# Performance work log

Hardware: AMD Instinct MI355X
Metric: run time of the kernel (lower is better)

Reference implementation:

```python
import jax, jax.numpy as jnp
from jax import lax
import numpy as np

B, S, N, F, H = 8, 64, 256, 16, 16
C = N * H  # temporal conv channels = 4096
ALPHA = 0.2
EPS = 1e-5
NEG = -9e15


def setup_inputs() -> dict:
    key = jax.random.key(0)
    ks = jax.random.split(key, 10)
    x = jax.random.normal(ks[0], (B, S, N, F), dtype=jnp.float32)
    adj = jax.random.normal(ks[1], (N, N), dtype=jnp.float32)
    W = jax.random.normal(ks[2], (F, H), dtype=jnp.float32) * (1.414 / np.sqrt(F))
    a = jax.random.normal(ks[3], (2 * H,), dtype=jnp.float32) * (1.414 / np.sqrt(2 * H))
    a1, a2 = a[:H], a[H:]
    conv_w = jax.random.normal(ks[4], (C, C, 3), dtype=jnp.float32) * (1.0 / np.sqrt(C * 3))
    conv_b = jnp.zeros((C,), dtype=jnp.float32)
    bn_gamma = jnp.ones((C,), dtype=jnp.float32)
    bn_beta = jnp.zeros((C,), dtype=jnp.float32)
    bn_mean = jnp.zeros((C,), dtype=jnp.float32)
    bn_var = jnp.ones((C,), dtype=jnp.float32)
    ln_gamma = jnp.ones((H,), dtype=jnp.float32)
    ln_beta = jnp.zeros((H,), dtype=jnp.float32)
    return {"x": x, "adj": adj, "W": W, "a1": a1, "a2": a2,
            "conv_w": conv_w, "conv_b": conv_b,
            "bn_gamma": bn_gamma, "bn_beta": bn_beta,
            "bn_mean": bn_mean, "bn_var": bn_var,
            "ln_gamma": ln_gamma, "ln_beta": ln_beta}


def reference(x, adj, W, a1, a2, conv_w, conv_b, bn_gamma, bn_beta, bn_mean, bn_var, ln_gamma, ln_beta):
    b, s, n, f = x.shape
    h = W.shape[1]
    # --- GAT, batched over all timesteps (eval mode: dropout is identity) ---
    Wh = jnp.einsum('bsnf,fh->bsnh', x, W)            # (B,S,N,H)
    # e_ij = LeakyReLU(a1.Wh_i + a2.Wh_j), equivalent to concat-then-matmul
    f1 = jnp.einsum('bsnh,h->bsn', Wh, a1)
    f2 = jnp.einsum('bsnh,h->bsn', Wh, a2)
    e = jax.nn.leaky_relu(f1[..., :, None] + f2[..., None, :], ALPHA)  # (B,S,N,N)
    e = jnp.where(adj > 0, e, NEG)
    attn = jax.nn.softmax(e, axis=-1)
    spatial = jnp.einsum('bsij,bsjh->bsih', attn, Wh)  # (B,S,N,H)
    # --- temporal conv over seq dim, channels = N*H ---
    t = spatial.reshape(b, s, n * h).transpose(0, 2, 1)  # (B,C,S)
    y = lax.conv_general_dilated(t, conv_w, window_strides=(1,), padding=[(1, 1)],
                                 dimension_numbers=('NCH', 'OIH', 'NCH'))
    y = y + conv_b[None, :, None]
    # BatchNorm1d in eval mode
    y = (y - bn_mean[None, :, None]) / jnp.sqrt(bn_var + EPS)[None, :, None]
    y = y * bn_gamma[None, :, None] + bn_beta[None, :, None]
    y = jax.nn.relu(y)
    temp = y.transpose(0, 2, 1).reshape(b, s, n, h)
    # residual is identity since in_features == hidden_dim
    out = temp + x
    # LayerNorm over last dim
    mu = out.mean(-1, keepdims=True)
    var = out.var(-1, keepdims=True)
    out = (out - mu) / jnp.sqrt(var + EPS) * ln_gamma + ln_beta
    return out
```

## Files before the change

kernel.cpp:

```cpp
#include <hip/hip_runtime.h>
#include <stdint.h>

#define ALPHA 0.2f
#define EPSV  1e-5f

typedef unsigned short u16;
typedef unsigned int   u32;
typedef unsigned long long u64;
typedef __bf16 bf16x8 __attribute__((ext_vector_type(8)));
typedef __bf16 bf16x2 __attribute__((ext_vector_type(2)));
typedef float  f32x4  __attribute__((ext_vector_type(4)));

#define NB 8
#define NS 64
#define NN 256
#define NF 16
#define NH 16
#define NC 4096
#define NK 12288
#define NP 512

__device__ __forceinline__ u16 f2b(float f){
  u32 u = __float_as_uint(f);
  u32 r = u + 0x7fffu + ((u>>16)&1u);
  return (u16)(r>>16);
}
__device__ __forceinline__ u32 pack2(float a, float b){ return (u32)f2b(a) | ((u32)f2b(b)<<16); }
__device__ __forceinline__ void un2(u32 v, float& lo, float& hi){
  lo = __uint_as_float(v<<16); hi = __uint_as_float(v & 0xffff0000u);
}
__device__ __forceinline__ void gld16(void* lds, const void* g){
  __builtin_amdgcn_global_load_lds((const __attribute__((address_space(1))) u32*)g,
                                   (__attribute__((address_space(3))) u32*)lds, 16, 0, 0);
}
__device__ __forceinline__ uint4 cvt8(f32x4 a, f32x4 b){
  union { uint4 u; bf16x2 h[4]; } r;
  r.h[0] = (bf16x2){(__bf16)a[0], (__bf16)a[1]};
  r.h[1] = (bf16x2){(__bf16)a[2], (__bf16)a[3]};
  r.h[2] = (bf16x2){(__bf16)b[0], (__bf16)b[1]};
  r.h[3] = (bf16x2){(__bf16)b[2], (__bf16)b[3]};
  return r.u;
}

__global__ __launch_bounds__(256) void k_adj(const float* __restrict__ adj,
                                             u64* __restrict__ am){
  int w = threadIdx.x>>6, l = threadIdx.x&63;
  int row = blockIdx.x*4 + w;
  #pragma unroll
  for(int g=0;g<4;g++){
    float v = adj[(size_t)row*NN + g*64 + l];
    u64 m = __ballot(v > 0.f);
    if(l==0) am[row*4+g] = m;
  }
}

__global__ __launch_bounds__(256) void k_attn(
    const float* __restrict__ x, const float* __restrict__ W,
    const float* __restrict__ a1, const float* __restrict__ a2,
    const u64* __restrict__ am, u16* __restrict__ Bt){
  __shared__ __align__(16) float Ws[NF][NH];
  __shared__ float a1s[NH], a2s[NH];
  __shared__ __align__(16) float Whs[NN][NH];
  __shared__ float f2s[NN];
  int t = threadIdx.x, bs = blockIdx.x;
  int b = bs>>6, s = bs&63;
  Ws[t>>4][t&15] = W[t];
  if(t<NH){ a1s[t]=a1[t]; a2s[t]=a2[t]; }
  u64 mg[4];
  #pragma unroll
  for(int g=0;g<4;g++) mg[g] = am[t*4+g];
  __syncthreads();

  const float* xp = x + ((size_t)bs*NN + t)*NF;
  float xr[16];
  #pragma unroll
  for(int g=0;g<4;g++) *(f32x4*)&xr[g*4] = ((const f32x4*)xp)[g];
  float wh[16];
  #pragma unroll
  for(int h=0;h<16;h++) wh[h]=0.f;
  #pragma unroll
  for(int f=0;f<16;f++){
    float xf = xr[f];
    #pragma unroll
    for(int h=0;h<16;h++) wh[h] = fmaf(xf, Ws[f][h], wh[h]);
  }
  float fi=0.f, s2=0.f;
  #pragma unroll
  for(int h=0;h<16;h++){ fi=fmaf(wh[h],a1s[h],fi); s2=fmaf(wh[h],a2s[h],s2); }
  #pragma unroll
  for(int g=0;g<4;g++) ((f32x4*)Whs[t])[g] = *(f32x4*)&wh[g*4];
  f2s[t] = s2;
  __syncthreads();

  float den = 0.f;
  f32x4 a0={0,0,0,0}, a1v={0,0,0,0}, a2v={0,0,0,0}, a3v={0,0,0,0};
  #pragma unroll
  for(int g=0;g<4;g++){
    u64 mm = mg[g];
    for(int jj=0;jj<64;jj++){
      int j = g*64+jj;
      float e = fi + f2s[j];
      e = e > 0.f ? e : ALPHA*e;
      float p = ((mm>>jj)&1ull) ? __expf(e) : 0.f;
      den += p;
      const f32x4* wr = (const f32x4*)Whs[j];
      a0 += wr[0]*p; a1v += wr[1]*p; a2v += wr[2]*p; a3v += wr[3]*p;
    }
  }
  float inv = 1.f/fmaxf(den, 1e-30f);
  float vals[16];
  *(f32x4*)&vals[0]  = a0*inv;  *(f32x4*)&vals[4]  = a1v*inv;
  *(f32x4*)&vals[8]  = a2v*inv; *(f32x4*)&vals[12] = a3v*inv;

  #pragma unroll
  for(int k=0;k<3;k++){
    int cs = s + 1 - k;
    if(cs >= 0 && cs < NS){
      size_t base = ((size_t)(b*NS+cs))*NK + (size_t)t*48 + k;
      #pragma unroll
      for(int h=0;h<16;h++) Bt[base + h*3] = f2b(vals[h]);
    }
  }
  if(s == 0){
    size_t base = ((size_t)(b*NS))*NK + (size_t)t*48;
    #pragma unroll
    for(int h=0;h<16;h++) Bt[base + h*3] = 0;
  }
  if(s == NS-1){
    size_t base = ((size_t)(b*NS+NS-1))*NK + (size_t)t*48 + 2;
    #pragma unroll
    for(int h=0;h<16;h++) Bt[base + h*3] = 0;
  }
}

__global__ __launch_bounds__(256) void k_gemm(
    const u16* __restrict__ Abt, const float* __restrict__ Bwf,
    u16* __restrict__ yp, int kchunk){
  __shared__ __align__(16) u16 As0[128*32];
  __shared__ __align__(16) u16 As1[128*32];
  __shared__ __align__(16) u16 Bs0[128*32];
  __shared__ __align__(16) u16 Bs1[128*32];
  int t = threadIdx.x;
  int id = blockIdx.x;
  int xr_ = id & 7, q0 = id >> 3;
  int mI = q0 & 3, nhi = q0 >> 2;
  int m0 = mI*128, n0 = (nhi*8 + xr_)*128;
  int kbeg = blockIdx.y*kchunk;
  f32x4 acc[4][4];
  #pragma unroll
  for(int i=0;i<4;i++)
    #pragma unroll
    for(int j=0;j<4;j++) acc[i][j] = (f32x4){0,0,0,0};

  int l = t&63, w = t>>6;
  int wm = (w&1)*64, wn = (w>>1)*64;
  int q = l>>4, r16 = l&15;

  int c0 = t, c1 = t+256;
  const u16*   ga0 = Abt + (size_t)(m0 + (c0>>2))*NK + (c0&3)*8;
  const u16*   ga1 = Abt + (size_t)(m0 + (c1>>2))*NK + (c1&3)*8;
  const float* gb0 = Bwf + (size_t)(n0 + (c0>>2))*NK + (c0&3)*8;
  const float* gb1 = Bwf + (size_t)(n0 + (c1>>2))*NK + (c1&3)*8;
  u16 *la00 = As0 + c0*8, *la01 = As0 + c1*8;
  u16 *la10 = As1 + c0*8, *la11 = As1 + c1*8;
  u16 *lb00 = Bs0 + c0*8, *lb01 = Bs0 + c1*8;
  u16 *lb10 = Bs1 + c0*8, *lb11 = Bs1 + c1*8;

  for(int kk=0; kk<kchunk; kk+=64){
    int k0 = kbeg + kk;
    f32x4 v00a = *(const f32x4*)(gb0 + k0);
    f32x4 v00b = *(const f32x4*)(gb0 + k0 + 4);
    f32x4 v01a = *(const f32x4*)(gb1 + k0);
    f32x4 v01b = *(const f32x4*)(gb1 + k0 + 4);
    f32x4 v10a = *(const f32x4*)(gb0 + k0 + 32);
    f32x4 v10b = *(const f32x4*)(gb0 + k0 + 36);
    f32x4 v11a = *(const f32x4*)(gb1 + k0 + 32);
    f32x4 v11b = *(const f32x4*)(gb1 + k0 + 36);
    uint4 w00 = cvt8(v00a, v00b);
    uint4 w01 = cvt8(v01a, v01b);
    uint4 w10 = cvt8(v10a, v10b);
    uint4 w11 = cvt8(v11a, v11b);
    __syncthreads();
    gld16(la00, ga0 + k0);      gld16(la01, ga1 + k0);
    gld16(la10, ga0 + k0 + 32); gld16(la11, ga1 + k0 + 32);
    *(uint4*)lb00 = w00; *(uint4*)lb01 = w01;
    *(uint4*)lb10 = w10; *(uint4*)lb11 = w11;
    __syncthreads();
    {
      bf16x8 af[4], bfr[4];
      #pragma unroll
      for(int mt=0;mt<4;mt++) af[mt]  = *(const bf16x8*)(As0 + (wm+mt*16+r16)*32 + q*8);
      #pragma unroll
      for(int nt=0;nt<4;nt++) bfr[nt] = *(const bf16x8*)(Bs0 + (wn+nt*16+r16)*32 + q*8);
      #pragma unroll
      for(int mt=0;mt<4;mt++)
        #pragma unroll
        for(int nt=0;nt<4;nt++)
          acc[mt][nt] = __builtin_amdgcn_mfma_f32_16x16x32_bf16(af[mt], bfr[nt], acc[mt][nt], 0,0,0);
    }
    {
      bf16x8 af[4], bfr[4];
      #pragma unroll
      for(int mt=0;mt<4;mt++) af[mt]  = *(const bf16x8*)(As1 + (wm+mt*16+r16)*32 + q*8);
      #pragma unroll
      for(int nt=0;nt<4;nt++) bfr[nt] = *(const bf16x8*)(Bs1 + (wn+nt*16+r16)*32 + q*8);
      #pragma unroll
      for(int mt=0;mt<4;mt++)
        #pragma unroll
        for(int nt=0;nt<4;nt++)
          acc[mt][nt] = __builtin_amdgcn_mfma_f32_16x16x32_bf16(af[mt], bfr[nt], acc[mt][nt], 0,0,0);
    }
  }
  u16* op = yp + (size_t)blockIdx.y*NP*NC;
  #pragma unroll
  for(int mt=0;mt<4;mt++)
    #pragma unroll
    for(int nt=0;nt<4;nt++)
      #pragma unroll
      for(int rr=0;rr<4;rr++){
        int m = m0 + wm + mt*16 + q*4 + rr;
        int n = n0 + wn + nt*16 + r16;
        op[(size_t)m*NC + n] = f2b(acc[mt][nt][rr]);
      }
}

__global__ __launch_bounds__(256) void k_post(
    const u16* __restrict__ yp, int nparts,
    const float* __restrict__ x,
    const float* __restrict__ cb, const float* __restrict__ bg,
    const float* __restrict__ bb, const float* __restrict__ bm,
    const float* __restrict__ bv, const float* __restrict__ lg,
    const float* __restrict__ lb, float* __restrict__ out){
  int n = threadIdx.x, bs = blockIdx.x;
  float v[16];
  #pragma unroll
  for(int h=0;h<16;h++) v[h]=0.f;
  for(int p=0;p<nparts;p++){
    const u16* pp = yp + (size_t)p*NP*NC + (size_t)bs*NC + n*16;
    uint4 u0 = ((const uint4*)pp)[0];
    uint4 u1 = ((const uint4*)pp)[1];
    float lo, hi;
    un2(u0.x,lo,hi); v[0]+=lo;  v[1]+=hi;
    un2(u0.y,lo,hi); v[2]+=lo;  v[3]+=hi;
    un2(u0.z,lo,hi); v[4]+=lo;  v[5]+=hi;
    un2(u0.w,lo,hi); v[6]+=lo;  v[7]+=hi;
    un2(u1.x,lo,hi); v[8]+=lo;  v[9]+=hi;
    un2(u1.y,lo,hi); v[10]+=lo; v[11]+=hi;
    un2(u1.z,lo,hi); v[12]+=lo; v[13]+=hi;
    un2(u1.w,lo,hi); v[14]+=lo; v[15]+=hi;
  }
  const float* xp = x + ((size_t)bs*NN + n)*NH;
  float xr[16];
  #pragma unroll
  for(int g=0;g<4;g++) *(f32x4*)&xr[g*4] = ((const f32x4*)xp)[g];

  float mu = 0.f;
  #pragma unroll
  for(int h=0;h<16;h++){
    int co = n*16 + h;
    float t1 = v[h] + cb[co];
    t1 = (t1 - bm[co]) * (1.f/sqrtf(bv[co] + EPSV));
    t1 = t1 * bg[co] + bb[co];
    t1 = fmaxf(t1, 0.f);
    t1 += xr[h];
    v[h] = t1; mu += t1;
  }
  mu *= (1.f/16.f);
  float var = 0.f;
  #pragma unroll
  for(int h=0;h<16;h++){ float d = v[h]-mu; var = fmaf(d,d,var); }
  var *= (1.f/16.f);
  float rs = 1.f/sqrtf(var + EPSV);
  float* op = out + ((size_t)bs*NN + n)*NH;
  #pragma unroll
  for(int h=0;h<16;h++) op[h] = (v[h]-mu)*rs*lg[h] + lb[h];
}

extern "C" void kernel_launch(void* const* d_in, const int* in_sizes, int n_in,
                              void* d_out, int out_size, void* d_ws, size_t ws_size,
                              hipStream_t stream){
  const float* x   = (const float*)d_in[0];
  const float* adj = (const float*)d_in[1];
  const float* W   = (const float*)d_in[2];
  const float* a1  = (const float*)d_in[3];
  const float* a2  = (const float*)d_in[4];
  const float* cw  = (const float*)d_in[5];
  const float* cb  = (const float*)d_in[6];
  const float* bg  = (const float*)d_in[7];
  const float* bb  = (const float*)d_in[8];
  const float* bm  = (const float*)d_in[9];
  const float* bv  = (const float*)d_in[10];
  const float* lg  = (const float*)d_in[11];
  const float* lb  = (const float*)d_in[12];
  float* out = (float*)d_out;

  char* ws = (char*)d_ws;
  const size_t AM_OFF = 0;
  const size_t BT_OFF = AM_OFF + (size_t)NN*4*8;
  const size_t YP_OFF = BT_OFF + (size_t)NP*NK*2;
  const size_t ypb    = (size_t)NP*NC*2;
  int P = 1;
  if(ws_size >= YP_OFF + 8*ypb)      P = 8;
  else if(ws_size >= YP_OFF + 4*ypb) P = 4;
  else if(ws_size >= YP_OFF + 2*ypb) P = 2;

  u64*   am  = (u64*)  (ws + AM_OFF);
  u16*   Bt  = (u16*)  (ws + BT_OFF);
  u16*   yp  = (u16*)  (ws + YP_OFF);

  hipLaunchKernelGGL(k_adj,  dim3(64),    dim3(256), 0, stream, adj, am);
  hipLaunchKernelGGL(k_attn, dim3(NP),    dim3(256), 0, stream, x,W,a1,a2,am,Bt);
  hipLaunchKernelGGL(k_gemm, dim3(128,P), dim3(256), 0, stream, Bt, cw, yp, NK/P);
  hipLaunchKernelGGL(k_post, dim3(NP),    dim3(256), 0, stream, yp,P,x,cb,bg,bb,bm,bv,lg,lb,out);
}
```

Before: 429.3 us.

## Pre-convert conv weights to bf16 and use padded spatial layout as implicit im2col

```diff
diff --git a/kernel.cpp b/kernel.cpp
--- a/kernel.cpp
+++ b/kernel.cpp
@@ -19,6 +19,7 @@
 #define NC 4096
 #define NK 12288
 #define NP 512
+#define SROW 66
 
 __device__ __forceinline__ u16 f2b(float f){
   u32 u = __float_as_uint(f);
@@ -43,7 +44,8 @@
 }
 
 __global__ __launch_bounds__(256) void k_adj(const float* __restrict__ adj,
-                                             u64* __restrict__ am){
+                                             u64* __restrict__ am,
+                                             uint4* __restrict__ spz){
   int w = threadIdx.x>>6, l = threadIdx.x&63;
   int row = blockIdx.x*4 + w;
   #pragma unroll
@@ -52,9 +54,181 @@
     u64 m = __ballot(v > 0.f);
     if(l==0) am[row*4+g] = m;
   }
+  if(spz){
+    int g = blockIdx.x*256 + threadIdx.x;
+    if(g < 8192){
+      int r = g>>9;
+      int b = r>>1;
+      size_t prow = (size_t)b*SROW + ((r&1) ? (SROW-1) : 0);
+      spz[prow*512 + (g&511)] = (uint4){0,0,0,0};
+    }
+  }
+}
+
+__global__ __launch_bounds__(256) void k_cw(const float* __restrict__ cw,
+                                            u16* __restrict__ Bw){
+  __shared__ __align__(16) float rs_[NK];
+  int t = threadIdx.x, co = blockIdx.x;
+  const float* src = cw + (size_t)co*NK;
+  #pragma unroll
+  for(int i=0;i<12;i++)
+    gld16(rs_ + (i*256 + t)*4, src + (i*256 + t)*4);
+  __syncthreads();
+  u16* dst = Bw + (size_t)co*NK;
+  #pragma unroll
+  for(int c=0;c<6;c++){
+    int o  = c*2048 + t*8;
+    int k  = o>>12, ci = o & 4095;
+    const float* p = rs_ + ci*3 + k;
+    union { uint4 u; u16 h[8]; } r;
+    #pragma unroll
+    for(int j=0;j<8;j++) r.h[j] = f2b(p[j*3]);
+    *(uint4*)(dst + o) = r.u;
+  }
 }
 
 __global__ __launch_bounds__(256) void k_attn(
+    const float* __restrict__ x, const float* __restrict__ W,
+    const float* __restrict__ a1, const float* __restrict__ a2,
+    const u64* __restrict__ am, u16* __restrict__ Sp){
+  __shared__ __align__(16) float Ws[NF][NH];
+  __shared__ float a1s[NH], a2s[NH];
+  __shared__ __align__(16) float Whs[NN][NH];
+  __shared__ float f2s[NN];
+  int t = threadIdx.x, bs = blockIdx.x;
+  int b = bs>>6, s = bs&63;
+  Ws[t>>4][t&15] = W[t];
+  if(t<NH){ a1s[t]=a1[t]; a2s[t]=a2[t]; }
+  u64 mg[4];
+  #pragma unroll
+  for(int g=0;g<4;g++) mg[g] = am[t*4+g];
+  __syncthreads();
+
+  const float* xp = x + ((size_t)bs*NN + t)*NF;
+  float xr[16];
+  #pragma unroll
+  for(int g=0;g<4;g++) *(f32x4*)&xr[g*4] = ((const f32x4*)xp)[g];
+  float wh[16];
+  #pragma unroll
+  for(int h=0;h<16;h++) wh[h]=0.f;
+  #pragma unroll
+  for(int f=0;f<16;f++){
+    float xf = xr[f];
+    #pragma unroll
+    for(int h=0;h<16;h++) wh[h] = fmaf(xf, Ws[f][h], wh[h]);
+  }
+  float fi=0.f, s2=0.f;
+  #pragma unroll
+  for(int h=0;h<16;h++){ fi=fmaf(wh[h],a1s[h],fi); s2=fmaf(wh[h],a2s[h],s2); }
+  #pragma unroll
+  for(int g=0;g<4;g++) ((f32x4*)Whs[t])[g] = *(f32x4*)&wh[g*4];
+  f2s[t] = s2;
+  __syncthreads();
+
+  float den = 0.f;
+  f32x4 a0={0,0,0,0}, a1v={0,0,0,0}, a2v={0,0,0,0}, a3v={0,0,0,0};
+  #pragma unroll
+  for(int g=0;g<4;g++){
+    u64 mm = mg[g];
+    for(int jj=0;jj<64;jj++){
+      int j = g*64+jj;
+      float e = fi + f2s[j];
+      e = e > 0.f ? e : ALPHA*e;
+      float p = ((mm>>jj)&1ull) ? __expf(e) : 0.f;
+      den += p;
+      const f32x4* wr = (const f32x4*)Whs[j];
+      a0 += wr[0]*p; a1v += wr[1]*p; a2v += wr[2]*p; a3v += wr[3]*p;
+    }
+  }
+  float inv = 1.f/fmaxf(den, 1e-30f);
+  f32x4 o0 = a0*inv, o1 = a1v*inv, o2 = a2v*inv, o3 = a3v*inv;
+
+  uint4 w0 = cvt8(o0,o1), w1 = cvt8(o2,o3);
+  uint4* op = (uint4*)(Sp + ((size_t)(b*SROW + s + 1))*NC) + t*2;
+  op[0] = w0; op[1] = w1;
+}
+
+__global__ __launch_bounds__(256) void k_gemm(
+    const u16* __restrict__ Asp, const u16* __restrict__ Bw,
+    u16* __restrict__ yp, int kchunk){
+  __shared__ __align__(16) u16 As0[128*32];
+  __shared__ __align__(16) u16 As1[128*32];
+  __shared__ __align__(16) u16 Bs0[128*32];
+  __shared__ __align__(16) u16 Bs1[128*32];
+  int t = threadIdx.x;
+  int id = blockIdx.x;
+  int xr_ = id & 7, q0 = id >> 3;
+  int mI = q0 & 3, nhi = q0 >> 2;
+  int m0 = mI*128, n0 = (nhi*8 + xr_)*128;
+  int kbeg = blockIdx.y*kchunk;
+  f32x4 acc[4][4];
+  #pragma unroll
+  for(int i=0;i<4;i++)
+    #pragma unroll
+    for(int j=0;j<4;j++) acc[i][j] = (f32x4){0,0,0,0};
+
+  int l = t&63, w = t>>6;
+  int wm = (w&1)*64, wn = (w>>1)*64;
+  int q = l>>4, r16 = l&15;
+
+  int c0 = t, c1 = t+256;
+  int mA0 = m0 + (c0>>2), mA1 = m0 + (c1>>2);
+  const u16* ga0 = Asp + (size_t)((mA0>>6)*SROW + (mA0&63))*NC + (c0&3)*8;
+  const u16* ga1 = Asp + (size_t)((mA1>>6)*SROW + (mA1&63))*NC + (c1&3)*8;
+  const u16* gb0 = Bw  + (size_t)(n0 + (c0>>2))*NK + (c0&3)*8;
+  const u16* gb1 = Bw  + (size_t)(n0 + (c1>>2))*NK + (c1&3)*8;
+  u16 *la00 = As0 + c0*8, *la01 = As0 + c1*8;
+  u16 *la10 = As1 + c0*8, *la11 = As1 + c1*8;
+  u16 *lb00 = Bs0 + c0*8, *lb01 = Bs0 + c1*8;
+  u16 *lb10 = Bs1 + c0*8, *lb11 = Bs1 + c1*8;
+
+  for(int kk=0; kk<kchunk; kk+=64){
+    int k0 = kbeg + kk;
+    __syncthreads();
+    gld16(la00, ga0 + k0);      gld16(la01, ga1 + k0);
+    gld16(la10, ga0 + k0 + 32); gld16(la11, ga1 + k0 + 32);
+    gld16(lb00, gb0 + k0);      gld16(lb01, gb1 + k0);
+    gld16(lb10, gb0 + k0 + 32); gld16(lb11, gb1 + k0 + 32);
+    __syncthreads();
+    {
+      bf16x8 af[4], bfr[4];
+      #pragma unroll
+      for(int mt=0;mt<4;mt++) af[mt]  = *(const bf16x8*)(As0 + (wm+mt*16+r16)*32 + q*8);
+      #pragma unroll
+      for(int nt=0;nt<4;nt++) bfr[nt] = *(const bf16x8*)(Bs0 + (wn+nt*16+r16)*32 + q*8);
+      #pragma unroll
+      for(int mt=0;mt<4;mt++)
+        #pragma unroll
+        for(int nt=0;nt<4;nt++)
+          acc[mt][nt] = __builtin_amdgcn_mfma_f32_16x16x32_bf16(af[mt], bfr[nt], acc[mt][nt], 0,0,0);
+    }
+    {
+      bf16x8 af[4], bfr[4];
+      #pragma unroll
+      for(int mt=0;mt<4;mt++) af[mt]  = *(const bf16x8*)(As1 + (wm+mt*16+r16)*32 + q*8);
+      #pragma unroll
+      for(int nt=0;nt<4;nt++) bfr[nt] = *(const bf16x8*)(Bs1 + (wn+nt*16+r16)*32 + q*8);
+      #pragma unroll
+      for(int mt=0;mt<4;mt++)
+        #pragma unroll
+        for(int nt=0;nt<4;nt++)
+          acc[mt][nt] = __builtin_amdgcn_mfma_f32_16x16x32_bf16(af[mt], bfr[nt], acc[mt][nt], 0,0,0);
+    }
+  }
+  u16* op = yp + (size_t)blockIdx.y*NP*NC;
+  #pragma unroll
+  for(int mt=0;mt<4;mt++)
+    #pragma unroll
+    for(int nt=0;nt<4;nt++)
+      #pragma unroll
+      for(int rr=0;rr<4;rr++){
+        int m = m0 + wm + mt*16 + q*4 + rr;
+        int n = n0 + wn + nt*16 + r16;
+        op[(size_t)m*NC + n] = f2b(acc[mt][nt][rr]);
+      }
+}
+
+__global__ __launch_bounds__(256) void k_attn_s(
     const float* __restrict__ x, const float* __restrict__ W,
     const float* __restrict__ a1, const float* __restrict__ a2,
     const u64* __restrict__ am, u16* __restrict__ Bt){
@@ -133,7 +307,7 @@
   }
 }
 
-__global__ __launch_bounds__(256) void k_gemm(
+__global__ __launch_bounds__(256) void k_gemm_f(
     const u16* __restrict__ Abt, const float* __restrict__ Bwf,
     u16* __restrict__ yp, int kchunk){
   __shared__ __align__(16) u16 As0[128*32];
@@ -295,21 +469,43 @@
   float* out = (float*)d_out;
 
   char* ws = (char*)d_ws;
-  const size_t AM_OFF = 0;
-  const size_t BT_OFF = AM_OFF + (size_t)NN*4*8;
-  const size_t YP_OFF = BT_OFF + (size_t)NP*NK*2;
-  const size_t ypb    = (size_t)NP*NC*2;
-  int P = 1;
-  if(ws_size >= YP_OFF + 8*ypb)      P = 8;
-  else if(ws_size >= YP_OFF + 4*ypb) P = 4;
-  else if(ws_size >= YP_OFF + 2*ypb) P = 2;
-
-  u64*   am  = (u64*)  (ws + AM_OFF);
-  u16*   Bt  = (u16*)  (ws + BT_OFF);
-  u16*   yp  = (u16*)  (ws + YP_OFF);
-
-  hipLaunchKernelGGL(k_adj,  dim3(64),    dim3(256), 0, stream, adj, am);
-  hipLaunchKernelGGL(k_attn, dim3(NP),    dim3(256), 0, stream, x,W,a1,a2,am,Bt);
-  hipLaunchKernelGGL(k_gemm, dim3(128,P), dim3(256), 0, stream, Bt, cw, yp, NK/P);
-  hipLaunchKernelGGL(k_post, dim3(NP),    dim3(256), 0, stream, yp,P,x,cb,bg,bb,bm,bv,lg,lb,out);
-}
+  const size_t ypb = (size_t)NP*NC*2;
+
+  const size_t SP_OFF  = 8192;
+  const size_t SP_SZ   = (size_t)NB*SROW*NC*2;
+  const size_t BW_OFF  = SP_OFF + SP_SZ;
+  const size_t BW_SZ   = (size_t)NC*NK*2;
+  const size_t YP_OFF2 = BW_OFF + BW_SZ;
+
+  u64* am = (u64*)ws;
+
+  int P2 = 0;
+  if(ws_size >= YP_OFF2 + 8*ypb)      P2 = 8;
+  else if(ws_size >= YP_OFF2 + 4*ypb) P2 = 4;
+  else if(ws_size >= YP_OFF2 + 2*ypb) P2 = 2;
+  else if(ws_size >= YP_OFF2 + 1*ypb) P2 = 1;
+
+  if(P2){
+    u16* Sp = (u16*)(ws + SP_OFF);
+    u16* Bw = (u16*)(ws + BW_OFF);
+    u16* yp = (u16*)(ws + YP_OFF2);
+    hipLaunchKernelGGL(k_adj,  dim3(64),      dim3(256), 0, stream, adj, am, (uint4*)Sp);
+    hipLaunchKernelGGL(k_cw,   dim3(NC),      dim3(256), 0, stream, cw, Bw);
+    hipLaunchKernelGGL(k_attn, dim3(NP),      dim3(256), 0, stream, x,W,a1,a2,am,Sp);
+    hipLaunchKernelGGL(k_gemm, dim3(128,P2),  dim3(256), 0, stream, Sp, Bw, yp, NK/P2);
+    hipLaunchKernelGGL(k_post, dim3(NP),      dim3(256), 0, stream, yp,P2,x,cb,bg,bb,bm,bv,lg,lb,out);
+  } else {
+    const size_t BT_OFF = 8192;
+    const size_t YP_OFF = BT_OFF + (size_t)NP*NK*2;
+    int P = 1;
+    if(ws_size >= YP_OFF + 8*ypb)      P = 8;
+    else if(ws_size >= YP_OFF + 4*ypb) P = 4;
+    else if(ws_size >= YP_OFF + 2*ypb) P = 2;
+    u16* Bt = (u16*)(ws + BT_OFF);
+    u16* yp = (u16*)(ws + YP_OFF);
+    hipLaunchKernelGGL(k_adj,    dim3(64),     dim3(256), 0, stream, adj, am, (uint4*)0);
+    hipLaunchKernelGGL(k_attn_s, dim3(NP),     dim3(256), 0, stream, x,W,a1,a2,am,Bt);
+    hipLaunchKernelGGL(k_gemm_f, dim3(128,P),  dim3(256), 0, stream, Bt, cw, yp, NK/P);
+    hipLaunchKernelGGL(k_post,   dim3(NP),     dim3(256), 0, stream, yp,P,x,cb,bg,bb,bm,bv,lg,lb,out);
+  }
+}
```

Result: slower. 449.1 us (+4.6%).
